# Kernel optimization log

Hardware: AMD Instinct MI355X
Metric: run time of the kernel (lower is better)

The kernel has to match this reference:

```python
import jax, jax.numpy as jnp
import numpy as np

B, S, D, H = 4, 2048, 1024, 16
HD = D // H

def setup_inputs() -> dict:
    key = jax.random.key(0)
    ks = jax.random.split(key, 5)
    x = jax.random.normal(ks[0], (B, S, D), dtype=jnp.float32)
    mask = jnp.ones((B, S), dtype=jnp.int32)
    # torch nn.Linear init scale ~ 1/sqrt(fan_in); use small normal for stability
    qkv_w = jax.random.normal(ks[1], (3 * D, D), dtype=jnp.float32) * (1.0 / np.sqrt(D))
    qkv_b = jax.random.normal(ks[2], (3 * D,), dtype=jnp.float32) * 0.02
    out_w = jax.random.normal(ks[3], (D, D), dtype=jnp.float32) * (1.0 / np.sqrt(D))
    out_b = jax.random.normal(ks[4], (D,), dtype=jnp.float32) * 0.02
    return {"x": x, "mask": mask, "qkv_w": qkv_w, "qkv_b": qkv_b,
            "out_w": out_w, "out_b": out_b}

def reference(x, mask, qkv_w, qkv_b, out_w, out_b):
    b, s, d = x.shape
    scale = np.sqrt(HD).astype(np.float32)
    # qkv projection: torch Linear y = x @ W^T + b
    qkv = x @ qkv_w.T + qkv_b                      # (b, s, 3d)
    qkv = qkv.reshape(b, s, 3, H, HD)
    qkv = jnp.transpose(qkv, (2, 0, 3, 1, 4))      # (3, b, H, s, hd)
    q, k, v = qkv[0], qkv[1], qkv[2]
    scores = jnp.einsum('bhqd,bhkd->bhqk', q, k) / scale  # (b, H, s, s)
    neg_inf = jnp.float32(-jnp.inf)
    causal = jnp.tril(jnp.ones((s, s), dtype=bool))
    scores = jnp.where(causal[None, None], scores, neg_inf)
    key_mask = (mask != 0)[:, None, None, :]       # (b, 1, 1, s)
    scores = jnp.where(key_mask, scores, neg_inf)
    attn = jax.nn.softmax(scores, axis=-1)
    out = jnp.einsum('bhqk,bhkd->bhqd', attn, v)   # (b, H, s, hd)
    out = jnp.transpose(out, (0, 2, 1, 3)).reshape(b, s, d)
    return out @ out_w.T + out_b
```

## Files before the change

kernel.cpp:

```cpp
#include <hip/hip_runtime.h>
#include <stdint.h>
#include <type_traits>

#define BB  4
#define SS  2048
#define DD  1024
#define HH  16
#define HDD 64

typedef __attribute__((ext_vector_type(8))) short s16x8;
typedef __attribute__((ext_vector_type(4))) float f32x4;

__device__ inline short f2bf(float f) {
    union { float f; unsigned int u; } v; v.f = f;
    unsigned int r = (v.u + 0x7fffu + ((v.u >> 16) & 1u)) >> 16;
    return (short)r;
}

__device__ inline float bf2f(short s) {
    union { unsigned int u; float f; } v;
    v.u = ((unsigned int)(unsigned short)s) << 16;
    return v.f;
}

__device__ inline unsigned int pk2(float a, float b) {
    return (unsigned int)(unsigned short)f2bf(a) |
           ((unsigned int)(unsigned short)f2bf(b) << 16);
}

#define GLL(gp, lp) __builtin_amdgcn_global_load_lds( \
    (const __attribute__((address_space(1))) void*)(gp), \
    (__attribute__((address_space(3))) void*)(lp), 16, 0, 0)

__device__ inline void lds_barrier() {
    asm volatile("s_waitcnt lgkmcnt(0)" ::: "memory");
    __builtin_amdgcn_sched_barrier(0);
    __builtin_amdgcn_s_barrier();
    __builtin_amdgcn_sched_barrier(0);
}

__global__ void cvt_all(const float* __restrict__ x, const float* __restrict__ qw,
                        const float* __restrict__ ow, short* __restrict__ dst) {
    const int X_N  = BB * SS * DD;
    const int QW_N = 3 * DD * DD;
    int i = (blockIdx.x * 256 + threadIdx.x) * 8;
    const float* s;
    if (i < X_N)            s = x + i;
    else if (i < X_N + QW_N) s = qw + (i - X_N);
    else                     s = ow + (i - X_N - QW_N);
    const float4* sp = (const float4*)s;
    float4 a = sp[0], b = sp[1];
    s16x8 o;
    o[0]=f2bf(a.x); o[1]=f2bf(a.y); o[2]=f2bf(a.z); o[3]=f2bf(a.w);
    o[4]=f2bf(b.x); o[5]=f2bf(b.y); o[6]=f2bf(b.z); o[7]=f2bf(b.w);
    *(s16x8*)(dst + i) = o;
}

template<int EPI>
__global__ __launch_bounds__(256, 2)
void gemm128(const short* __restrict__ A, const short* __restrict__ Bw,
             const float* __restrict__ bias, float* __restrict__ Cf,
             short* __restrict__ Qo, short* __restrict__ Ko, short* __restrict__ Vo,
             int M, int N, int K, int nbx)
{
    __shared__ short lsA[2][128 * 64];
    __shared__ short lsB[2][128 * 64];

    const int tid  = threadIdx.x;
    const int w    = tid >> 6, lane = tid & 63;
    const int quad = lane >> 4, l15 = lane & 15;
    const int wm = w >> 1, wn = w & 1;
    const int cpx = gridDim.x >> 3;
    const int swz = (blockIdx.x & 7) * cpx + (blockIdx.x >> 3);
    const int m0 = (swz / nbx) * 128, n0 = (swz % nbx) * 128;
    const int grow = lane >> 3;
    const int gcol = ((lane & 7) ^ grow) * 8;
    const int l7 = l15 & 7;

    f32x4 acc[4][4] = {};

    auto issue = [&](int kt, int buf) {
#pragma unroll
        for (int jj = 0; jj < 4; ++jj) {
            int row = w * 32 + jj * 8 + grow;
            GLL(A + (size_t)(m0 + row) * K + kt * 64 + gcol,
                &lsA[buf][(w * 4 + jj) * 512]);
        }
#pragma unroll
        for (int jj = 0; jj < 4; ++jj) {
            int row = w * 32 + jj * 8 + grow;
            GLL(Bw + (size_t)(n0 + row) * K + kt * 64 + gcol,
                &lsB[buf][(w * 4 + jj) * 512]);
        }
    };

    const int NT = K >> 6;
    issue(0, 0);
    for (int t = 0; t < NT; ++t) {
        const int buf = t & 1;
        lds_barrier();
        if (t + 1 < NT) {
            issue(t + 1, buf ^ 1);
            asm volatile("s_waitcnt vmcnt(8)" ::: "memory");
        } else {
            asm volatile("s_waitcnt vmcnt(0)" ::: "memory");
        }
        __builtin_amdgcn_sched_barrier(0);
        __builtin_amdgcn_s_barrier();
        __builtin_amdgcn_sched_barrier(0);

        s16x8 af[4][2], bfr[4][2];
#pragma unroll
        for (int mf = 0; mf < 4; ++mf)
#pragma unroll
            for (int ks = 0; ks < 2; ++ks)
                af[mf][ks] = *(const s16x8*)&lsA[buf][(wm * 64 + mf * 16 + l15) * 64 +
                                                     (((ks * 4 + quad) ^ l7) * 8)];
#pragma unroll
        for (int nf = 0; nf < 4; ++nf)
#pragma unroll
            for (int ks = 0; ks < 2; ++ks)
                bfr[nf][ks] = *(const s16x8*)&lsB[buf][(wn * 64 + nf * 16 + l15) * 64 +
                                                      (((ks * 4 + quad) ^ l7) * 8)];

        __builtin_amdgcn_s_setprio(1);
#pragma unroll
        for (int ks = 0; ks < 2; ++ks)
#pragma unroll
            for (int mf = 0; mf < 4; ++mf)
#pragma unroll
                for (int nf = 0; nf < 4; ++nf)
                    acc[mf][nf] = __builtin_amdgcn_mfma_f32_16x16x32_bf16(
                                      af[mf][ks], bfr[nf][ks], acc[mf][nf], 0, 0, 0);
        __builtin_amdgcn_s_setprio(0);
    }

    if (EPI == 0) {
#pragma unroll
        for (int mf = 0; mf < 4; ++mf) {
            int row = m0 + wm * 64 + mf * 16 + quad * 4;
#pragma unroll
            for (int nf = 0; nf < 4; ++nf) {
                int col = n0 + wn * 64 + nf * 16 + l15;
                float bv = bias[col];
#pragma unroll
                for (int r = 0; r < 4; ++r)
                    Cf[(size_t)(row + r) * N + col] = acc[mf][nf][r] + bv;
            }
        }
    } else {
#pragma unroll
        for (int mf = 0; mf < 4; ++mf) {
            int row = m0 + wm * 64 + mf * 16 + quad * 4;
#pragma unroll
            for (int nf = 0; nf < 4; ++nf) {
                int col = n0 + wn * 64 + nf * 16 + l15;
                float bv = bias[col];
                int sel = col >> 10, h = (col >> 6) & 15, hd = col & 63;
#pragma unroll
                for (int r = 0; r < 4; ++r) {
                    int rr = row + r;
                    int b = rr >> 11, s = rr & 2047;
                    short val = f2bf(acc[mf][nf][r] + bv);
                    if (sel == 0)      Qo[(((size_t)b * HH + h) * SS + s) * HDD + hd] = val;
                    else if (sel == 1) Ko[(((size_t)b * HH + h) * SS + s) * HDD + hd] = val;
                    else               Vo[(((size_t)b * HH + h) * HDD + hd) * SS + s] = val;
                }
            }
        }
    }
}

__global__ __launch_bounds__(256, 2)
void attn_kernel(const short* __restrict__ Q, const short* __restrict__ Kb,
                 const short* __restrict__ Vb, const int* __restrict__ mask,
                 short* __restrict__ O)
{
    __shared__ short lsK[2][64 * 64];
    __shared__ short lsV[2][64 * 64];
    __shared__ short lsP[4][32 * 64];
    __shared__ short lsM[SS];

    const int tid  = threadIdx.x;
    const int w    = tid >> 6, lane = tid & 63;
    const int quad = lane >> 4, l15 = lane & 15;
    const int L  = blockIdx.x + 8 * blockIdx.y;
    const int bx = L >> 6;
    const int bh = (L & 7) * 8 + ((L >> 3) & 7);
    const int b = bh >> 4;
    const size_t baseQK = (size_t)bh * SS * HDD;
    const size_t baseV  = (size_t)bh * HDD * SS;
    const float SC = 0.18033688f;
    const int grow = lane >> 3;
    const int gcol = ((lane & 7) ^ grow) * 8;
    const int l7 = l15 & 7;

    {
        const int4* mp = (const int4*)(mask + b * SS);
        int4 a = mp[tid * 2], c = mp[tid * 2 + 1];
        const short NEG = f2bf(-1e30f);
        s16x8 mo;
        mo[0] = a.x ? (short)0 : NEG; mo[1] = a.y ? (short)0 : NEG;
        mo[2] = a.z ? (short)0 : NEG; mo[3] = a.w ? (short)0 : NEG;
        mo[4] = c.x ? (short)0 : NEG; mo[5] = c.y ? (short)0 : NEG;
        mo[6] = c.z ? (short)0 : NEG; mo[7] = c.w ? (short)0 : NEG;
        *(s16x8*)&lsM[tid * 8] = mo;
    }

    auto issue = [&](int kv0, int buf) {
#pragma unroll
        for (int jj = 0; jj < 2; ++jj) {
            int row = w * 16 + jj * 8 + grow;
            GLL(Kb + baseQK + (size_t)(kv0 + row) * HDD + gcol,
                &lsK[buf][(w * 2 + jj) * 512]);
        }
#pragma unroll
        for (int jj = 0; jj < 2; ++jj) {
            int row = w * 16 + jj * 8 + grow;
            GLL(Vb + baseV + (size_t)row * SS + kv0 + gcol,
                &lsV[buf][(w * 2 + jj) * 512]);
        }
    };

    for (int t = 0; t < 2; ++t) {
        const int qb = t ? bx : (15 - bx);
        const int q0 = qb * 128;
        const int qw0 = q0 + w * 32;

        s16x8 aq[2][2];
#pragma unroll
        for (int s = 0; s < 2; ++s)
#pragma unroll
            for (int ks = 0; ks < 2; ++ks)
                aq[s][ks] = *(const s16x8*)(Q + baseQK +
                    (size_t)(qw0 + s * 16 + l15) * HDD + ks * 32 + quad * 8);

        float m_r[2], l_r[2];
        f32x4 o_acc[2][4] = {};
#pragma unroll
        for (int s = 0; s < 2; ++s) { m_r[s] = -1e30f; l_r[s] = 0.f; }

        const int ntiles = 2 * qb + 2;

        lds_barrier();
        issue(0, 0);

        auto tile = [&](auto CC, int kv0, int buf, int kvn) {
            constexpr bool CAUS = decltype(CC)::value;

            lds_barrier();
            if (kvn >= 0) issue(kvn, buf ^ 1);

            float madd[4][4];
#pragma unroll
            for (int nt = 0; nt < 4; ++nt) {
                uint2 mw4 = *(const uint2*)&lsM[kv0 + nt * 16 + quad * 4];
                madd[nt][0] = bf2f((short)(mw4.x & 0xffff));
                madd[nt][1] = bf2f((short)(mw4.x >> 16));
                madd[nt][2] = bf2f((short)(mw4.y & 0xffff));
                madd[nt][3] = bf2f((short)(mw4.y >> 16));
            }

            if (kvn >= 0) asm volatile("s_waitcnt vmcnt(4)" ::: "memory");
            else          asm volatile("s_waitcnt vmcnt(0)" ::: "memory");
            __builtin_amdgcn_sched_barrier(0);
            __builtin_amdgcn_s_barrier();
            __builtin_amdgcn_sched_barrier(0);

            f32x4 sv[2][4];
#pragma unroll
            for (int s = 0; s < 2; ++s)
#pragma unroll
                for (int nt = 0; nt < 4; ++nt) sv[s][nt] = f32x4{};
#pragma unroll
            for (int ks = 0; ks < 2; ++ks)
#pragma unroll
                for (int nt = 0; nt < 4; ++nt) {
                    s16x8 kf = *(const s16x8*)&lsK[buf][(nt * 16 + l15) * 64 +
                                                       (((ks * 4 + quad) ^ l7) * 8)];
#pragma unroll
                    for (int s = 0; s < 2; ++s)
                        sv[s][nt] = __builtin_amdgcn_mfma_f32_16x16x32_bf16(
                                        kf, aq[s][ks], sv[s][nt], 0, 0, 0);
                }

#pragma unroll
            for (int s = 0; s < 2; ++s) {
                const int qg = qw0 + s * 16 + l15;
#pragma unroll
                for (int nt = 0; nt < 4; ++nt) {
                    const int kg0 = kv0 + nt * 16 + quad * 4;
#pragma unroll
                    for (int r = 0; r < 4; ++r) {
                        float scv = sv[s][nt][r] * SC + madd[nt][r];
                        if (CAUS && kg0 + r > qg) scv = -1e30f;
                        sv[s][nt][r] = scv;
                    }
                }
            }

            float rm[2];
#pragma unroll
            for (int s = 0; s < 2; ++s) {
                float v = fmaxf(fmaxf(fmaxf(sv[s][0][0], sv[s][0][1]),
                                      fmaxf(sv[s][0][2], sv[s][0][3])),
                                fmaxf(fmaxf(sv[s][1][0], sv[s][1][1]),
                                      fmaxf(sv[s][1][2], sv[s][1][3])));
                float v2 = fmaxf(fmaxf(fmaxf(sv[s][2][0], sv[s][2][1]),
                                       fmaxf(sv[s][2][2], sv[s][2][3])),
                                 fmaxf(fmaxf(sv[s][3][0], sv[s][3][1]),
                                       fmaxf(sv[s][3][2], sv[s][3][3])));
                v = fmaxf(v, v2);
                v = fmaxf(v, __shfl_xor(v, 16));
                v = fmaxf(v, __shfl_xor(v, 32));
                rm[s] = v;
            }
            float need = fmaxf(rm[0] - m_r[0], rm[1] - m_r[1]);
            if (!__all(need <= 8.0f)) {
#pragma unroll
                for (int s = 0; s < 2; ++s) {
                    float nm = fmaxf(m_r[s], rm[s]);
                    float al = __builtin_amdgcn_exp2f(m_r[s] - nm);
                    m_r[s] = nm;
                    l_r[s] *= al;
#pragma unroll
                    for (int r = 0; r < 4; ++r) {
                        float alq = __shfl(al, (quad << 2) + r + (lane & 48));
#pragma unroll
                        for (int ht = 0; ht < 4; ++ht)
                            o_acc[s][ht][r] *= alq;
                    }
                }
            }
#pragma unroll
            for (int s = 0; s < 2; ++s) {
                float rs = 0.f;
#pragma unroll
                for (int nt = 0; nt < 4; ++nt)
#pragma unroll
                    for (int r = 0; r < 4; ++r) {
                        float p = __builtin_amdgcn_exp2f(sv[s][nt][r] - m_r[s]);
                        sv[s][nt][r] = p;
                        rs += p;
                    }
                l_r[s] += rs;
            }

            short* lsPw = lsP[w];
#pragma unroll
            for (int s = 0; s < 2; ++s)
#pragma unroll
                for (int nt = 0; nt < 4; ++nt) {
                    uint2 pw;
                    pw.x = pk2(sv[s][nt][0], sv[s][nt][1]);
                    pw.y = pk2(sv[s][nt][2], sv[s][nt][3]);
                    int row = s * 16 + l15;
                    int g8 = (nt * 2 + (quad >> 1)) ^ l7;
                    *(uint2*)&lsPw[row * 64 + (g8 << 3) + ((quad & 1) << 2)] = pw;
                }
            asm volatile("s_waitcnt lgkmcnt(0)" ::: "memory");
            __builtin_amdgcn_sched_barrier(0);

            s16x8 ap[2][2];
#pragma unroll
            for (int s = 0; s < 2; ++s)
#pragma unroll
                for (int k2 = 0; k2 < 2; ++k2)
                    ap[s][k2] = *(const s16x8*)&lsPw[(s * 16 + l15) * 64 +
                                                     (((k2 * 4 + quad) ^ l7) << 3)];
#pragma unroll
            for (int ht = 0; ht < 4; ++ht)
#pragma unroll
                for (int k2 = 0; k2 < 2; ++k2) {
                    s16x8 vf = *(const s16x8*)&lsV[buf][(ht * 16 + l15) * 64 +
                                                        (((k2 * 4 + quad) ^ l7) * 8)];
#pragma unroll
                    for (int s = 0; s < 2; ++s)
                        o_acc[s][ht] = __builtin_amdgcn_mfma_f32_16x16x32_bf16(
                                           ap[s][k2], vf, o_acc[s][ht], 0, 0, 0);
                }
        };

        for (int kt = 0; kt < ntiles; ++kt) {
            const int kvn = (kt + 1 < ntiles) ? (kt + 1) * 64 : -1;
            if (kt >= 2 * qb) tile(std::true_type{},  kt * 64, kt & 1, kvn);
            else              tile(std::false_type{}, kt * 64, kt & 1, kvn);
        }

        const int hcol = (bh & 15) * HDD;
#pragma unroll
        for (int s = 0; s < 2; ++s) {
            float ls = l_r[s];
            ls += __shfl_xor(ls, 16);
            ls += __shfl_xor(ls, 32);
#pragma unroll
            for (int r = 0; r < 4; ++r) {
                float lq = __shfl(ls, (quad << 2) + r + (lane & 48));
                float inv = 1.0f / lq;
                int srow = qw0 + s * 16 + quad * 4 + r;
                size_t base = ((size_t)b * SS + srow) * DD + hcol;
#pragma unroll
                for (int ht = 0; ht < 4; ++ht)
                    O[base + ht * 16 + l15] = f2bf(o_acc[s][ht][r] * inv);
            }
        }
    }
}

extern "C" void kernel_launch(void* const* d_in, const int* in_sizes, int n_in,
                              void* d_out, int out_size, void* d_ws, size_t ws_size,
                              hipStream_t stream) {
    const float* x     = (const float*)d_in[0];
    const int*   mask  = (const int*)d_in[1];
    const float* qkv_w = (const float*)d_in[2];
    const float* qkv_b = (const float*)d_in[3];
    const float* out_w = (const float*)d_in[4];
    const float* out_b = (const float*)d_in[5];
    float* out = (float*)d_out;

    const size_t M1 = (size_t)BB * SS;
    short* ws  = (short*)d_ws;
    short* xb  = ws;
    short* qwb = xb  + M1 * DD;
    short* owb = qwb + (size_t)3 * DD * DD;
    short* Qb  = owb + (size_t)DD * DD;
    short* Kb  = Qb  + M1 * DD;
    short* Vb  = Kb  + M1 * DD;
    short* Ob  = Vb  + M1 * DD;

    cvt_all<<<6144, 256, 0, stream>>>(x, qkv_w, out_w, ws);

    gemm128<1><<<1536, 256, 0, stream>>>(xb, qwb, qkv_b, nullptr,
                                         Qb, Kb, Vb, 8192, 3072, 1024, 24);
    attn_kernel<<<dim3(8, BB * HH), 256, 0, stream>>>(Qb, Kb, Vb, mask, Ob);
    gemm128<0><<<512, 256, 0, stream>>>(Ob, owb, out_b, out,
                                        nullptr, nullptr, nullptr, 8192, 1024, 1024, 8);
}
```

Baseline: 284.8 us.

## Switch GEMM to triple-buffered BK=32 pipeline with prefetch distance two

```diff
diff --git a/kernel.cpp b/kernel.cpp
--- a/kernel.cpp
+++ b/kernel.cpp
@@ -57,14 +57,14 @@
 }
 
 template<int EPI>
-__global__ __launch_bounds__(256, 2)
-void gemm128(const short* __restrict__ A, const short* __restrict__ Bw,
-             const float* __restrict__ bias, float* __restrict__ Cf,
-             short* __restrict__ Qo, short* __restrict__ Ko, short* __restrict__ Vo,
-             int M, int N, int K, int nbx)
+__global__ __launch_bounds__(256, 3)
+void gemm128tb(const short* __restrict__ A, const short* __restrict__ Bw,
+               const float* __restrict__ bias, float* __restrict__ Cf,
+               short* __restrict__ Qo, short* __restrict__ Ko, short* __restrict__ Vo,
+               int M, int N, int K, int nbx)
 {
-    __shared__ short lsA[2][128 * 64];
-    __shared__ short lsB[2][128 * 64];
+    __shared__ short lsA[3][128 * 32];
+    __shared__ short lsB[3][128 * 32];
 
     const int tid  = threadIdx.x;
     const int w    = tid >> 6, lane = tid & 63;
@@ -73,35 +73,39 @@
     const int cpx = gridDim.x >> 3;
     const int swz = (blockIdx.x & 7) * cpx + (blockIdx.x >> 3);
     const int m0 = (swz / nbx) * 128, n0 = (swz % nbx) * 128;
-    const int grow = lane >> 3;
-    const int gcol = ((lane & 7) ^ grow) * 8;
-    const int l7 = l15 & 7;
+    const int grow = lane >> 2;
+    const int gcol = ((lane & 3) ^ (grow & 3)) * 8;
+    const int rsw = (l15 & 3);
 
     f32x4 acc[4][4] = {};
 
     auto issue = [&](int kt, int buf) {
 #pragma unroll
-        for (int jj = 0; jj < 4; ++jj) {
-            int row = w * 32 + jj * 8 + grow;
-            GLL(A + (size_t)(m0 + row) * K + kt * 64 + gcol,
-                &lsA[buf][(w * 4 + jj) * 512]);
-        }
-#pragma unroll
-        for (int jj = 0; jj < 4; ++jj) {
-            int row = w * 32 + jj * 8 + grow;
-            GLL(Bw + (size_t)(n0 + row) * K + kt * 64 + gcol,
-                &lsB[buf][(w * 4 + jj) * 512]);
+        for (int jj = 0; jj < 2; ++jj) {
+            int c = w * 2 + jj;
+            GLL(A + (size_t)(m0 + c * 16 + grow) * K + kt * 32 + gcol,
+                &lsA[buf][c * 512]);
+        }
+#pragma unroll
+        for (int jj = 0; jj < 2; ++jj) {
+            int c = w * 2 + jj;
+            GLL(Bw + (size_t)(n0 + c * 16 + grow) * K + kt * 32 + gcol,
+                &lsB[buf][c * 512]);
         }
     };
 
-    const int NT = K >> 6;
+    const int NT = K >> 5;
     issue(0, 0);
+    issue(1, 1);
+    int buf = 0;
     for (int t = 0; t < NT; ++t) {
-        const int buf = t & 1;
         lds_barrier();
-        if (t + 1 < NT) {
-            issue(t + 1, buf ^ 1);
+        const int nb2 = (buf + 2 >= 3) ? buf - 1 : buf + 2;
+        if (t + 2 < NT) {
+            issue(t + 2, nb2);
             asm volatile("s_waitcnt vmcnt(8)" ::: "memory");
+        } else if (t + 1 < NT) {
+            asm volatile("s_waitcnt vmcnt(4)" ::: "memory");
         } else {
             asm volatile("s_waitcnt vmcnt(0)" ::: "memory");
         }
@@ -109,30 +113,26 @@
         __builtin_amdgcn_s_barrier();
         __builtin_amdgcn_sched_barrier(0);
 
-        s16x8 af[4][2], bfr[4][2];
+        s16x8 af[4], bfr[4];
 #pragma unroll
         for (int mf = 0; mf < 4; ++mf)
-#pragma unroll
-            for (int ks = 0; ks < 2; ++ks)
-                af[mf][ks] = *(const s16x8*)&lsA[buf][(wm * 64 + mf * 16 + l15) * 64 +
-                                                     (((ks * 4 + quad) ^ l7) * 8)];
+            af[mf] = *(const s16x8*)&lsA[buf][(wm * 64 + mf * 16 + l15) * 32 +
+                                             ((quad ^ rsw) * 8)];
 #pragma unroll
         for (int nf = 0; nf < 4; ++nf)
-#pragma unroll
-            for (int ks = 0; ks < 2; ++ks)
-                bfr[nf][ks] = *(const s16x8*)&lsB[buf][(wn * 64 + nf * 16 + l15) * 64 +
-                                                      (((ks * 4 + quad) ^ l7) * 8)];
+            bfr[nf] = *(const s16x8*)&lsB[buf][(wn * 64 + nf * 16 + l15) * 32 +
+                                              ((quad ^ rsw) * 8)];
 
         __builtin_amdgcn_s_setprio(1);
 #pragma unroll
-        for (int ks = 0; ks < 2; ++ks)
-#pragma unroll
-            for (int mf = 0; mf < 4; ++mf)
-#pragma unroll
-                for (int nf = 0; nf < 4; ++nf)
-                    acc[mf][nf] = __builtin_amdgcn_mfma_f32_16x16x32_bf16(
-                                      af[mf][ks], bfr[nf][ks], acc[mf][nf], 0, 0, 0);
+        for (int mf = 0; mf < 4; ++mf)
+#pragma unroll
+            for (int nf = 0; nf < 4; ++nf)
+                acc[mf][nf] = __builtin_amdgcn_mfma_f32_16x16x32_bf16(
+                                  af[mf], bfr[nf], acc[mf][nf], 0, 0, 0);
         __builtin_amdgcn_s_setprio(0);
+
+        buf = (buf + 1 >= 3) ? 0 : buf + 1;
     }
 
     if (EPI == 0) {
@@ -430,9 +430,9 @@
 
     cvt_all<<<6144, 256, 0, stream>>>(x, qkv_w, out_w, ws);
 
-    gemm128<1><<<1536, 256, 0, stream>>>(xb, qwb, qkv_b, nullptr,
-                                         Qb, Kb, Vb, 8192, 3072, 1024, 24);
+    gemm128tb<1><<<1536, 256, 0, stream>>>(xb, qwb, qkv_b, nullptr,
+                                           Qb, Kb, Vb, 8192, 3072, 1024, 24);
     attn_kernel<<<dim3(8, BB * HH), 256, 0, stream>>>(Qb, Kb, Vb, mask, Ob);
-    gemm128<0><<<512, 256, 0, stream>>>(Ob, owb, out_b, out,
-                                        nullptr, nullptr, nullptr, 8192, 1024, 1024, 8);
-}
+    gemm128tb<0><<<512, 256, 0, stream>>>(Ob, owb, out_b, out,
+                                          nullptr, nullptr, nullptr, 8192, 1024, 1024, 8);
+}
```

After: 284.4 us. No clear change (-0.1%).
